# Optimization experiments

Measured on AMD Instinct MI355X. Metric: run time of the kernel, lower is better.

The kernel has to match this reference:

```python
import jax, jax.numpy as jnp
import numpy as np

NUM_LABELS = 10  # number of distinct label values in the minibatch
EPS = 1e-8


def setup_inputs() -> dict:
    key = jax.random.key(0)
    k1, k2 = jax.random.split(key)
    z = jax.random.normal(k1, (8192, 20, 256), dtype=jnp.float32)  # [B, C, H]
    labels = jax.random.randint(k2, (8192,), 0, NUM_LABELS)  # [B]
    return {"z": z, "labels": labels}


def reference(z, labels):
    # CODI minibatch loss, positive pairs, representation space.
    # Equivalent to: for each unique label, mse(z[group] + 1e-8, mean(z[group]))
    # summed over labels. Vectorized as a single segment-mean +
    # gather-broadcast + segment-SSE pass (one traversal of z).
    z = jnp.nan_to_num(z)
    B, C, H = z.shape
    counts = jax.ops.segment_sum(
        jnp.ones((B,), dtype=z.dtype), labels, num_segments=NUM_LABELS
    )  # [K]
    sums = jax.ops.segment_sum(z, labels, num_segments=NUM_LABELS)  # [K, C, H]
    means = jnp.nan_to_num(sums / jnp.maximum(counts, 1.0)[:, None, None])
    # per-sample squared distance to its group's mean (note the +EPS as in torch)
    d = (z + EPS) - means[labels]  # [B, C, H]
    per_sample = jnp.sum(d * d, axis=(1, 2))  # [B]
    sse = jax.ops.segment_sum(per_sample, labels, num_segments=NUM_LABELS)  # [K]
    # nn.MSELoss is a mean over all elements of the group: count_k * C * H
    mse_k = sse / (jnp.maximum(counts, 1.0) * (C * H))
    # torch.unique only visits labels present in the batch -> mask empty groups
    return jnp.sum(jnp.where(counts > 0, jnp.nan_to_num(mse_k), 0.0))
```

## Files before the change

### kernel.cpp

```cpp
#include <hip/hip_runtime.h>

#define B_SZ   8192
#define CH     5120
#define CH4    1280
#define K_LAB  10
#define EPS    1e-8f
#define FLTMAX 3.402823466e38f

#define NTHR   256
#define NCHUNK 5
#define PS     32
#define PF     8


__global__ __launch_bounds__(640) void codi_setup(
    const int* __restrict__ labels, int* __restrict__ idx,
    int* __restrict__ off, float* __restrict__ SSQ, float* __restrict__ nsq)
{
    __shared__ int lab_s[B_SZ];
    __shared__ int cnts[K_LAB];
    __shared__ int offs[K_LAB + 1];
    const int tid  = threadIdx.x;
    const int k    = tid >> 6;
    const int lane = tid & 63;

    const int4* l4 = (const int4*)labels;
    for (int i = tid; i < B_SZ / 4; i += 640) ((int4*)lab_s)[i] = l4[i];
    __syncthreads();

    int cnt = 0;
    for (int b0 = 0; b0 < B_SZ; b0 += 64)
        cnt += __popcll(__ballot(lab_s[b0 + lane] == k));
    if (lane == 0) cnts[k] = cnt;
    __syncthreads();
    if (tid == 0) {
        int a = 0;
        for (int j = 0; j < K_LAB; ++j) { offs[j] = a; a += cnts[j]; }
        offs[K_LAB] = a;
    }
    __syncthreads();

    int base = offs[k];
    const unsigned long long ltmask = (1ULL << lane) - 1ULL;
    for (int b0 = 0; b0 < B_SZ; b0 += 64) {
        int lab = lab_s[b0 + lane];
        unsigned long long m = __ballot(lab == k);
        if (lab == k) idx[base + __popcll(m & ltmask)] = b0 + lane;
        base += __popcll(m);
    }
    if (tid < K_LAB + 1) off[tid] = offs[tid];
    if (tid < K_LAB) { SSQ[tid] = 0.f; nsq[tid] = 0.f; }
}

__global__ __launch_bounds__(NTHR) void codi_gather(
    const float4* __restrict__ z4, const int* __restrict__ idx,
    const int* __restrict__ off, float4* __restrict__ S_part,
    float* __restrict__ SSQ)
{
    const int tid   = threadIdx.x;
    const int k     = blockIdx.x / (NCHUNK * PS);
    const int rem   = blockIdx.x % (NCHUNK * PS);
    const int chunk = rem % NCHUNK;
    const int ps    = rem / NCHUNK;

    const int kb  = off[k];
    const int cnt = off[k + 1] - kb;
    const int s0  = kb + (int)(((long long)cnt * ps) / PS);
    const int s1  = kb + (int)(((long long)cnt * (ps + 1)) / PS);
    const int n   = s1 - s0;

    __shared__ int rows[288];
    for (int i = tid; i < n; i += NTHR) rows[i] = idx[s0 + i];
    __syncthreads();

    const int col4 = chunk * NTHR + tid;
    float4 sum = make_float4(0.f, 0.f, 0.f, 0.f);
    float  ssq = 0.f;

#define SANITIZE(v) do { \
        v.x = (v.x == v.x) ? fminf(fmaxf(v.x, -FLTMAX), FLTMAX) : 0.f; \
        v.y = (v.y == v.y) ? fminf(fmaxf(v.y, -FLTMAX), FLTMAX) : 0.f; \
        v.z = (v.z == v.z) ? fminf(fmaxf(v.z, -FLTMAX), FLTMAX) : 0.f; \
        v.w = (v.w == v.w) ? fminf(fmaxf(v.w, -FLTMAX), FLTMAX) : 0.f; \
    } while (0)
#define ACCUM(v) do { \
        sum.x += v.x; sum.y += v.y; sum.z += v.z; sum.w += v.w; \
        ssq = fmaf(v.x, v.x, ssq); ssq = fmaf(v.y, v.y, ssq); \
        ssq = fmaf(v.z, v.z, ssq); ssq = fmaf(v.w, v.w, ssq); \
    } while (0)

    const int n_main = n & ~(PF - 1);
    for (int i0 = 0; i0 < n_main; i0 += PF) {
        float4 vb[PF];
        #pragma unroll
        for (int u = 0; u < PF; ++u)
            vb[u] = z4[(size_t)rows[i0 + u] * CH4 + col4];
        #pragma unroll
        for (int u = 0; u < PF; ++u) { SANITIZE(vb[u]); ACCUM(vb[u]); }
    }
    if (n_main < n) {
        float4 vb[PF];
        #pragma unroll
        for (int u = 0; u < PF; ++u)
            if (n_main + u < n) vb[u] = z4[(size_t)rows[n_main + u] * CH4 + col4];
        #pragma unroll
        for (int u = 0; u < PF; ++u)
            if (n_main + u < n) { SANITIZE(vb[u]); ACCUM(vb[u]); }
    }
#undef SANITIZE
#undef ACCUM

    S_part[((size_t)(k * PS + ps)) * CH4 + col4] = sum;

    #pragma unroll
    for (int o = 32; o > 0; o >>= 1) ssq += __shfl_down(ssq, o, 64);
    if ((tid & 63) == 0) atomicAdd(&SSQ[k], ssq);
}

__global__ __launch_bounds__(NTHR) void codi_reduce(
    const float* __restrict__ S_part, float* __restrict__ nsq)
{
    const int i = blockIdx.x * NTHR + threadIdx.x;
    const int k = i / CH;
    const int c = i - k * CH;
    float s = 0.f;
    #pragma unroll
    for (int ps = 0; ps < PS; ++ps)
        s += S_part[((size_t)(k * PS + ps)) * CH + c];
    float w = s * s;
    #pragma unroll
    for (int o = 32; o > 0; o >>= 1) w += __shfl_down(w, o, 64);
    if ((threadIdx.x & 63) == 0) atomicAdd(&nsq[k], w);
}

__global__ __launch_bounds__(64) void codi_final(
    const int* __restrict__ off, const float* __restrict__ SSQ,
    const float* __restrict__ nsq, float* __restrict__ out)
{
    if (threadIdx.x == 0) {
        float loss = 0.f;
        for (int k = 0; k < K_LAB; ++k) {
            float n = (float)(off[k + 1] - off[k]);
            if (n > 0.f) {
                float sse = SSQ[k] - nsq[k] / n + n * (float)CH * (EPS * EPS);
                float mse = sse / (n * (float)CH);
                if (mse == mse) loss += mse;
            }
        }
        out[0] = loss;
    }
}

extern "C" void kernel_launch(void* const* d_in, const int* in_sizes, int n_in,
                              void* d_out, int out_size, void* d_ws, size_t ws_size,
                              hipStream_t stream) {
    const float4* z4     = (const float4*)d_in[0];
    const int*    labels = (const int*)d_in[1];

    float* hdr    = (float*)d_ws;
    float* SSQ    = hdr;
    float* nsq    = hdr + 16;
    int*   off    = (int*)(hdr + 32);
    int*   idx    = (int*)(hdr + 64);
    float* S_part = hdr + 64 + B_SZ;

    codi_setup<<<1, 640, 0, stream>>>(labels, idx, off, SSQ, nsq);
    codi_gather<<<K_LAB * NCHUNK * PS, NTHR, 0, stream>>>(
        z4, idx, off, (float4*)S_part, SSQ);
    codi_reduce<<<(K_LAB * CH) / NTHR, NTHR, 0, stream>>>(S_part, nsq);
    codi_final<<<1, 64, 0, stream>>>(off, SSQ, nsq, (float*)d_out);
}
```

Measured before the change: 301.2 us.

## Have each gather block cover full rows and vectorize the partial-sum reduce

The gather kernel now assigns one block of 320 threads to a full 5120-float row: each thread loads four float4 columns per row, three rows at a time, instead of five separate blocks each reading one column chunk. There are now 64 sample partitions per label, giving 640 blocks. The reduce kernel becomes float4-vectorized with 40 blocks that each sum 64 partials. The aim is to cut per-block overhead and duplicated index loading, and to get more bytes in flight per thread. In exchange the gather grid and the reduce grid are much smaller, which may underuse the GPU's CUs and lower memory-level parallelism. The partial buffer also doubles in size.

Result: faster. 279.1 us (-7.3%).

```diff
diff --git a/kernel.cpp b/kernel.cpp
--- a/kernel.cpp
+++ b/kernel.cpp
@@ -7,10 +7,9 @@
 #define EPS    1e-8f
 #define FLTMAX 3.402823466e38f
 
-#define NTHR   256
-#define NCHUNK 5
-#define PS     32
-#define PF     8
+#define NTHR   320
+#define PS     64
+#define RB     3
 
 
 __global__ __launch_bounds__(640) void codi_setup(
@@ -57,11 +56,9 @@
     const int* __restrict__ off, float4* __restrict__ S_part,
     float* __restrict__ SSQ)
 {
-    const int tid   = threadIdx.x;
-    const int k     = blockIdx.x / (NCHUNK * PS);
-    const int rem   = blockIdx.x % (NCHUNK * PS);
-    const int chunk = rem % NCHUNK;
-    const int ps    = rem / NCHUNK;
+    const int tid = threadIdx.x;
+    const int k   = blockIdx.x / PS;
+    const int ps  = blockIdx.x % PS;
 
     const int kb  = off[k];
     const int cnt = off[k + 1] - kb;
@@ -69,13 +66,14 @@
     const int s1  = kb + (int)(((long long)cnt * (ps + 1)) / PS);
     const int n   = s1 - s0;
 
-    __shared__ int rows[288];
+    __shared__ int rows[160];
     for (int i = tid; i < n; i += NTHR) rows[i] = idx[s0 + i];
     __syncthreads();
 
-    const int col4 = chunk * NTHR + tid;
-    float4 sum = make_float4(0.f, 0.f, 0.f, 0.f);
-    float  ssq = 0.f;
+    float4 sum[4];
+    #pragma unroll
+    for (int j = 0; j < 4; ++j) sum[j] = make_float4(0.f, 0.f, 0.f, 0.f);
+    float ssq = 0.f;
 
 #define SANITIZE(v) do { \
         v.x = (v.x == v.x) ? fminf(fmaxf(v.x, -FLTMAX), FLTMAX) : 0.f; \
@@ -83,34 +81,41 @@
         v.z = (v.z == v.z) ? fminf(fmaxf(v.z, -FLTMAX), FLTMAX) : 0.f; \
         v.w = (v.w == v.w) ? fminf(fmaxf(v.w, -FLTMAX), FLTMAX) : 0.f; \
     } while (0)
-#define ACCUM(v) do { \
-        sum.x += v.x; sum.y += v.y; sum.z += v.z; sum.w += v.w; \
+#define ACCUM(j, v) do { \
+        sum[j].x += v.x; sum[j].y += v.y; sum[j].z += v.z; sum[j].w += v.w; \
         ssq = fmaf(v.x, v.x, ssq); ssq = fmaf(v.y, v.y, ssq); \
         ssq = fmaf(v.z, v.z, ssq); ssq = fmaf(v.w, v.w, ssq); \
     } while (0)
 
-    const int n_main = n & ~(PF - 1);
-    for (int i0 = 0; i0 < n_main; i0 += PF) {
-        float4 vb[PF];
+    const int n_main = n - (n % RB);
+    for (int i0 = 0; i0 < n_main; i0 += RB) {
+        float4 vb[RB][4];
         #pragma unroll
-        for (int u = 0; u < PF; ++u)
-            vb[u] = z4[(size_t)rows[i0 + u] * CH4 + col4];
+        for (int u = 0; u < RB; ++u) {
+            const size_t rbase = (size_t)rows[i0 + u] * CH4;
+            #pragma unroll
+            for (int j = 0; j < 4; ++j)
+                vb[u][j] = z4[rbase + j * NTHR + tid];
+        }
         #pragma unroll
-        for (int u = 0; u < PF; ++u) { SANITIZE(vb[u]); ACCUM(vb[u]); }
+        for (int u = 0; u < RB; ++u)
+            #pragma unroll
+            for (int j = 0; j < 4; ++j) { SANITIZE(vb[u][j]); ACCUM(j, vb[u][j]); }
     }
-    if (n_main < n) {
-        float4 vb[PF];
+    for (int i = n_main; i < n; ++i) {
+        const size_t rbase = (size_t)rows[i] * CH4;
+        float4 vb[4];
         #pragma unroll
-        for (int u = 0; u < PF; ++u)
-            if (n_main + u < n) vb[u] = z4[(size_t)rows[n_main + u] * CH4 + col4];
+        for (int j = 0; j < 4; ++j) vb[j] = z4[rbase + j * NTHR + tid];
         #pragma unroll
-        for (int u = 0; u < PF; ++u)
-            if (n_main + u < n) { SANITIZE(vb[u]); ACCUM(vb[u]); }
+        for (int j = 0; j < 4; ++j) { SANITIZE(vb[j]); ACCUM(j, vb[j]); }
     }
 #undef SANITIZE
 #undef ACCUM
 
-    S_part[((size_t)(k * PS + ps)) * CH4 + col4] = sum;
+    float4* sp = S_part + (size_t)blockIdx.x * CH4;
+    #pragma unroll
+    for (int j = 0; j < 4; ++j) sp[j * NTHR + tid] = sum[j];
 
     #pragma unroll
     for (int o = 32; o > 0; o >>= 1) ssq += __shfl_down(ssq, o, 64);
@@ -118,19 +123,21 @@
 }
 
 __global__ __launch_bounds__(NTHR) void codi_reduce(
-    const float* __restrict__ S_part, float* __restrict__ nsq)
+    const float4* __restrict__ S_part, float* __restrict__ nsq)
 {
-    const int i = blockIdx.x * NTHR + threadIdx.x;
-    const int k = i / CH;
-    const int c = i - k * CH;
-    float s = 0.f;
-    #pragma unroll
-    for (int ps = 0; ps < PS; ++ps)
-        s += S_part[((size_t)(k * PS + ps)) * CH + c];
-    float w = s * s;
+    const int tid = threadIdx.x;
+    const int k   = blockIdx.x >> 2;
+    const int cc  = blockIdx.x & 3;
+    float4 s = make_float4(0.f, 0.f, 0.f, 0.f);
+    #pragma unroll 8
+    for (int ps = 0; ps < PS; ++ps) {
+        float4 v = S_part[((size_t)(k * PS + ps)) * CH4 + cc * NTHR + tid];
+        s.x += v.x; s.y += v.y; s.z += v.z; s.w += v.w;
+    }
+    float w = fmaf(s.x, s.x, fmaf(s.y, s.y, fmaf(s.z, s.z, s.w * s.w)));
     #pragma unroll
     for (int o = 32; o > 0; o >>= 1) w += __shfl_down(w, o, 64);
-    if ((threadIdx.x & 63) == 0) atomicAdd(&nsq[k], w);
+    if ((tid & 63) == 0) atomicAdd(&nsq[k], w);
 }
 
 __global__ __launch_bounds__(64) void codi_final(
@@ -165,8 +172,8 @@
     float* S_part = hdr + 64 + B_SZ;
 
     codi_setup<<<1, 640, 0, stream>>>(labels, idx, off, SSQ, nsq);
-    codi_gather<<<K_LAB * NCHUNK * PS, NTHR, 0, stream>>>(
+    codi_gather<<<K_LAB * PS, NTHR, 0, stream>>>(
         z4, idx, off, (float4*)S_part, SSQ);
-    codi_reduce<<<(K_LAB * CH) / NTHR, NTHR, 0, stream>>>(S_part, nsq);
+    codi_reduce<<<K_LAB * 4, NTHR, 0, stream>>>((const float4*)S_part, nsq);
     codi_final<<<1, 64, 0, stream>>>(off, SSQ, nsq, (float*)d_out);
 }
```
